# Performance work log

Measured on AMD Instinct MI355X. Metric: run time of the kernel, lower is better.

The kernel has to match this reference:

```python
import jax, jax.numpy as jnp
import numpy as np

B, S, HID = 2, 1024, 2048
N_HEADS, N_KV, HEAD_DIM = 32, 4, 128
BLOCK, MAX_BLOCKS = 32, 128
EPS = 1e-6
ROPE_THETA = 1e6


def _rmsnorm(x, w):
    # per-head RMSNorm over head_dim (Qwen3MoeRMSNorm)
    var = jnp.mean(x * x, axis=-1, keepdims=True)
    return x * jax.lax.rsqrt(var + EPS) * w


def _rotate_half(x):
    h = x.shape[-1] // 2
    return jnp.concatenate([-x[..., h:], x[..., :h]], axis=-1)


def setup_inputs() -> dict:
    key = jax.random.key(0)
    ks = jax.random.split(key, 8)
    hidden_states = jax.random.normal(ks[0], (B, S, HID), dtype=jnp.float32)
    wq = jax.random.normal(ks[1], (N_HEADS * HEAD_DIM, HID), dtype=jnp.float32) * 0.02
    wk = jax.random.normal(ks[2], (N_KV * HEAD_DIM, HID), dtype=jnp.float32) * 0.02
    wv = jax.random.normal(ks[3], (N_KV * HEAD_DIM, HID), dtype=jnp.float32) * 0.02
    wo = jax.random.normal(ks[4], (HID, N_HEADS * HEAD_DIM), dtype=jnp.float32) * 0.02
    q_norm_w = 1.0 + 0.01 * jax.random.normal(ks[5], (HEAD_DIM,), dtype=jnp.float32)
    k_norm_w = 1.0 + 0.01 * jax.random.normal(ks[6], (HEAD_DIM,), dtype=jnp.float32)
    # RoPE tables (rotate-half / llama convention)
    inv_freq = 1.0 / (ROPE_THETA ** (jnp.arange(0, HEAD_DIM, 2, dtype=jnp.float32) / HEAD_DIM))
    t = jnp.arange(S, dtype=jnp.float32)
    freqs = jnp.outer(t, inv_freq)  # [S, HEAD_DIM/2]
    emb = jnp.concatenate([freqs, freqs], axis=-1)  # [S, HEAD_DIM]
    cos, sin = jnp.cos(emb), jnp.sin(emb)
    # page table: B sequences x (S/BLOCK) blocks, distinct block ids
    page_table = jnp.arange(B * (S // BLOCK), dtype=jnp.int32).reshape(B, S // BLOCK)
    return {"hidden_states": hidden_states, "wq": wq, "wk": wk, "wv": wv, "wo": wo,
            "q_norm_w": q_norm_w, "k_norm_w": k_norm_w, "cos": cos, "sin": sin,
            "page_table": page_table}


def reference(hidden_states, wq, wk, wv, wo, q_norm_w, k_norm_w, cos, sin, page_table):
    b, s, _ = hidden_states.shape
    # fused QKV projection (math-equivalent to the concatenated qkv_proj_weight)
    q = (hidden_states @ wq.T).reshape(b, s, N_HEADS, HEAD_DIM)
    k = (hidden_states @ wk.T).reshape(b, s, N_KV, HEAD_DIM)
    v = (hidden_states @ wv.T).reshape(b, s, N_KV, HEAD_DIM)
    # per-head RMSNorm then RoPE
    q = _rmsnorm(q, q_norm_w)
    k = _rmsnorm(k, k_norm_w)
    c = cos[None, :, None, :]
    sn = sin[None, :, None, :]
    q = q * c + _rotate_half(q) * sn
    k = k * c + _rotate_half(k) * sn
    # paged KV-cache fill: [B, nblk, BLOCK, kvh, hd] -> cache[block_id, kvh, BLOCK, hd]
    nblk = s // BLOCK
    k_blk = k.reshape(b, nblk, BLOCK, N_KV, HEAD_DIM).transpose(0, 1, 3, 2, 4).reshape(-1, N_KV, BLOCK, HEAD_DIM)
    v_blk = v.reshape(b, nblk, BLOCK, N_KV, HEAD_DIM).transpose(0, 1, 3, 2, 4).reshape(-1, N_KV, BLOCK, HEAD_DIM)
    flat_pt = page_table.reshape(-1)
    cache_k = jnp.zeros((MAX_BLOCKS, N_KV, BLOCK, HEAD_DIM), dtype=k.dtype).at[flat_pt].set(k_blk)
    cache_v = jnp.zeros((MAX_BLOCKS, N_KV, BLOCK, HEAD_DIM), dtype=v.dtype).at[flat_pt].set(v_blk)
    # GQA: repeat kv heads (num_key_value_groups = 8)
    groups = N_HEADS // N_KV
    k_rep = jnp.repeat(k, groups, axis=2)  # [b, s, N_HEADS, hd]
    v_rep = jnp.repeat(v, groups, axis=2)
    # causal SDPA, scaling = head_dim ** -0.5
    scale = HEAD_DIM ** -0.5
    scores = jnp.einsum('bqhd,bkhd->bhqk', q, k_rep) * scale
    causal = jnp.tril(jnp.ones((s, s), dtype=bool))
    scores = jnp.where(causal[None, None], scores, jnp.finfo(scores.dtype).min)
    probs = jax.nn.softmax(scores, axis=-1)
    attn = jnp.einsum('bhqk,bkhd->bqhd', probs, v_rep).reshape(b, s, N_HEADS * HEAD_DIM)
    out = attn @ wo.T  # [b, s, HID]
    return out, cache_k, cache_v
```

## Files before the change

### kernel.cpp

```cpp
#include <hip/hip_runtime.h>
#include <hip/hip_bf16.h>


typedef __attribute__((ext_vector_type(8))) __bf16 bf16x8;
typedef __attribute__((ext_vector_type(4))) __bf16 bf16x4;
typedef __attribute__((ext_vector_type(4))) float f32x4;

__device__ __forceinline__ void gload16(const void* g, void* l) {
    __builtin_amdgcn_global_load_lds((const __attribute__((address_space(1))) void*)g,
                                     (__attribute__((address_space(3))) void*)l, 16, 0, 0);
}

__global__ __launch_bounds__(256) void cvt5(const float* __restrict__ s0, const float* __restrict__ s1,
                                            const float* __restrict__ s2, const float* __restrict__ s3,
                                            const float* __restrict__ s4,
                                            __bf16* __restrict__ d0, __bf16* __restrict__ d1,
                                            __bf16* __restrict__ d2, __bf16* __restrict__ d3,
                                            __bf16* __restrict__ d4) {
    const int b = blockIdx.x;
    const float* src; __bf16* dst; int off;
    if (b < 4096)       { src = s0; dst = d0; off = b; }
    else if (b < 12288) { src = s1; dst = d1; off = b - 4096; }
    else if (b < 13312) { src = s2; dst = d2; off = b - 12288; }
    else if (b < 14336) { src = s3; dst = d3; off = b - 13312; }
    else                { src = s4; dst = d4; off = b - 14336; }
    const int i = off * 256 + threadIdx.x;
    float4 v = reinterpret_cast<const float4*>(src)[i];
    bf16x4 o = {(__bf16)v.x, (__bf16)v.y, (__bf16)v.z, (__bf16)v.w};
    reinterpret_cast<bf16x4*>(dst)[i] = o;
}

__global__ __launch_bounds__(256) void reduce_add(float* __restrict__ o,
                                                  const float* __restrict__ p, int n4) {
    int i = blockIdx.x * 256 + threadIdx.x;
    int stride = gridDim.x * 256;
    for (; i < n4; i += stride) {
        float4 a = reinterpret_cast<float4*>(o)[i];
        float4 b = reinterpret_cast<const float4*>(p)[i];
        a.x += b.x; a.y += b.y; a.z += b.z; a.w += b.w;
        reinterpret_cast<float4*>(o)[i] = a;
    }
}

template <int NF, int OUT_BF16>
__global__ __launch_bounds__(512, 2) void gemm4p(const __bf16* __restrict__ A,
                                                 const __bf16* __restrict__ B,
                                                 void* __restrict__ C0,
                                                 void* __restrict__ C1,
                                                 const int M, const int N, const int K,
                                                 const int nTiles, const int nbn,
                                                 const int klen) {
    __shared__ __bf16 Asm[2 * 128 * 64];
    __shared__ __bf16 Bsm[2 * NF * 64 * 64];
    const int tid = threadIdx.x, lane = tid & 63, wave = tid >> 6;
    const int wm = wave >> 2, wn = wave & 3;
    const int lrow = lane & 15, lkg = lane >> 4;
    const int rsw = lrow & 7;
    const int bid = blockIdx.x;
    const int kz = bid / nTiles, tile = bid % nTiles;
    const int tswz = (tile & 7) * (nTiles >> 3) + (tile >> 3);
    const int bm = tswz / nbn, bn = tswz % nbn;
    const int brow = bm * 128, bcol = bn * (NF * 64);
    const int kbeg = kz * klen;
    const int row0 = tid >> 3;
    const int scol_sw = ((tid & 7) ^ (row0 & 7)) * 8;
    const __bf16* gA = A + (size_t)(brow + row0) * K + kbeg + scol_sw;
    const __bf16* gB = B + (size_t)(bcol + row0) * K + kbeg + scol_sw;
    const int slot0 = (lkg ^ rsw) * 8;
    const int slot1 = ((4 + lkg) ^ rsw) * 8;
    const int nt = klen / 64;
    constexpr int UPT = NF + 2;

    f32x4 acc[4][NF] = {};

    int su_t = 0, su_w = 0;
    auto stage1 = [&]() {
        if (su_t < nt) {
            const size_t ko = (size_t)su_t * 64;
            if (su_w < 2)
                gload16(gA + (size_t)(su_w * 64) * K + ko,
                        Asm + (su_t & 1) * 8192 + su_w * 4096 + tid * 8);
            else
                gload16(gB + (size_t)((su_w - 2) * 64) * K + ko,
                        Bsm + (su_t & 1) * (NF * 4096) + (su_w - 2) * 4096 + tid * 8);
        }
        if (++su_w == UPT) { su_w = 0; ++su_t; }
    };

    for (int u = 0; u < 2 * UPT; ++u) stage1();
    if constexpr (NF == 5) asm volatile("s_waitcnt vmcnt(7)" ::: "memory");
    else                   asm volatile("s_waitcnt vmcnt(6)" ::: "memory");
    __builtin_amdgcn_s_barrier();

    for (int t = 0; t < nt; ++t) {
        const __bf16* As = Asm + (t & 1) * 8192;
        const __bf16* Bs = Bsm + (t & 1) * (NF * 4096);
        bf16x8 ar[4], br[NF];
#pragma unroll
        for (int mi = 0; mi < 4; ++mi)
            ar[mi] = *reinterpret_cast<const bf16x8*>(&As[(wm * 64 + mi * 16 + lrow) * 64 + slot0]);
#pragma unroll
        for (int nf = 0; nf < NF; ++nf)
            br[nf] = *reinterpret_cast<const bf16x8*>(&Bs[(wn * (NF * 16) + nf * 16 + lrow) * 64 + slot0]);
        asm volatile("s_waitcnt lgkmcnt(0)" ::: "memory");
        __builtin_amdgcn_sched_barrier(0);
        __builtin_amdgcn_s_setprio(1);
#pragma unroll
        for (int mi = 0; mi < 4; ++mi)
#pragma unroll
            for (int nf = 0; nf < NF; ++nf)
                acc[mi][nf] = __builtin_amdgcn_mfma_f32_16x16x32_bf16(ar[mi], br[nf], acc[mi][nf], 0, 0, 0);
        __builtin_amdgcn_s_setprio(0);
        __builtin_amdgcn_s_barrier();
#pragma unroll
        for (int mi = 0; mi < 4; ++mi)
            ar[mi] = *reinterpret_cast<const bf16x8*>(&As[(wm * 64 + mi * 16 + lrow) * 64 + slot1]);
#pragma unroll
        for (int nf = 0; nf < NF; ++nf)
            br[nf] = *reinterpret_cast<const bf16x8*>(&Bs[(wn * (NF * 16) + nf * 16 + lrow) * 64 + slot1]);
        asm volatile("s_waitcnt lgkmcnt(0)" ::: "memory");
#pragma unroll
        for (int u = 0; u < UPT; ++u) stage1();
        __builtin_amdgcn_sched_barrier(0);
        __builtin_amdgcn_s_setprio(1);
#pragma unroll
        for (int mi = 0; mi < 4; ++mi)
#pragma unroll
            for (int nf = 0; nf < NF; ++nf)
                acc[mi][nf] = __builtin_amdgcn_mfma_f32_16x16x32_bf16(ar[mi], br[nf], acc[mi][nf], 0, 0, 0);
        __builtin_amdgcn_s_setprio(0);
        if (t + 2 < nt) {
            if constexpr (NF == 5) asm volatile("s_waitcnt vmcnt(7)" ::: "memory");
            else                   asm volatile("s_waitcnt vmcnt(6)" ::: "memory");
        } else {
            asm volatile("s_waitcnt vmcnt(0)" ::: "memory");
        }
        __builtin_amdgcn_s_barrier();
    }

    void* C = (kz == 0) ? C0 : C1;
#pragma unroll
    for (int mi = 0; mi < 4; ++mi)
#pragma unroll
        for (int nf = 0; nf < NF; ++nf)
#pragma unroll
            for (int j = 0; j < 4; ++j) {
                const size_t r = brow + wm * 64 + mi * 16 + lkg * 4 + j;
                const size_t c = bcol + wn * (NF * 16) + nf * 16 + lrow;
                if (OUT_BF16)
                    ((__bf16*)C)[r * N + c] = (__bf16)acc[mi][nf][j];
                else
                    ((float*)C)[r * N + c] = acc[mi][nf][j];
            }
}

__global__ __launch_bounds__(256) void norm_rope_cache(
    __bf16* __restrict__ qkv, const float* __restrict__ cosT, const float* __restrict__ sinT,
    const float* __restrict__ qw, const float* __restrict__ kw,
    const int* __restrict__ ptab, float* __restrict__ cacheK, float* __restrict__ cacheV) {
    const int t = blockIdx.x;
    const int b = t >> 10, s = t & 1023;
    const int wave = threadIdx.x >> 6, lane = threadIdx.x & 63;
    __bf16* row = qkv + (size_t)t * 5120;
    const float c = cosT[s * 128 + lane];
    const float sn = sinT[s * 128 + lane];
    const int page = ptab[b * 32 + (s >> 5)];
    const int so = s & 31;
    const float wq0 = qw[lane], wq1 = qw[lane + 64];
#pragma unroll
    for (int i = 0; i < 8; ++i) {
        const int h = wave * 8 + i;
        float x0 = (float)row[h * 128 + lane];
        float x1 = (float)row[h * 128 + 64 + lane];
        float ss = x0 * x0 + x1 * x1;
        for (int off = 32; off; off >>= 1) ss += __shfl_xor(ss, off);
        const float rs = rsqrtf(ss * (1.0f / 128.0f) + 1e-6f);
        const float y0 = x0 * rs * wq0, y1 = x1 * rs * wq1;
        row[h * 128 + lane]      = (__bf16)(y0 * c - y1 * sn);
        row[h * 128 + 64 + lane] = (__bf16)(y1 * c + y0 * sn);
    }
    {
        const int h = wave;
        float x0 = (float)row[4096 + h * 128 + lane];
        float x1 = (float)row[4096 + h * 128 + 64 + lane];
        float ss = x0 * x0 + x1 * x1;
        for (int off = 32; off; off >>= 1) ss += __shfl_xor(ss, off);
        const float rs = rsqrtf(ss * (1.0f / 128.0f) + 1e-6f);
        const float y0 = x0 * rs * kw[lane], y1 = x1 * rs * kw[lane + 64];
        const float o0 = y0 * c - y1 * sn, o1 = y1 * c + y0 * sn;
        row[4096 + h * 128 + lane]      = (__bf16)o0;
        row[4096 + h * 128 + 64 + lane] = (__bf16)o1;
        float* ck = cacheK + (((size_t)page * 4 + h) * 32 + so) * 128;
        ck[lane] = o0; ck[lane + 64] = o1;
        const float v0 = (float)row[4608 + h * 128 + lane];
        const float v1 = (float)row[4608 + h * 128 + 64 + lane];
        float* cv = cacheV + (((size_t)page * 4 + h) * 32 + so) * 128;
        cv[lane] = v0; cv[lane + 64] = v1;
    }
}

__global__ __launch_bounds__(512, 2) void attn_fwd(const __bf16* __restrict__ qkv,
                                                   __bf16* __restrict__ out) {
    __shared__ __bf16 Ks[2][128 * 128];
    __shared__ __bf16 Vs[128 * 128];
    __shared__ __bf16 Ps[8][2][16 * 64];
    const int bid = blockIdx.x;
    const int qa = bid >> 3;
    const int g = bid & 7;
    const int kvg = g & 3, b = g >> 2;
    const int qbig = 63 - qa;
    const int tid = threadIdx.x, wave = tid >> 6, lane = tid & 63;
    const int lrow = lane & 15, lkg = lane >> 4;
    const int h = kvg * 8 + wave;
    const size_t base = (size_t)b * 1024 * 5120;
    const int kofs = 4096 + kvg * 128, vofs = 4608 + kvg * 128;
    const int ntA = qa / 8 + 1, nt = qbig / 8 + 1;
    const int lastA = qa >> 2, lastB = qbig >> 2;
    const int qposA = qa * 16 + lrow, qposB = qbig * 16 + lrow;
    const int rsw = lrow & 7;
    constexpr float QS = 0.08838834764831845f * 1.4426950408889634f;
    constexpr float SUB = 20.0f;

    bf16x8 aqA[4], aqB[4];
#pragma unroll
    for (int kc = 0; kc < 4; ++kc) {
        bf16x8 ta = *reinterpret_cast<const bf16x8*>(
            &qkv[base + (size_t)(qa * 16 + lrow) * 5120 + h * 128 + kc * 32 + lkg * 8]);
        bf16x8 tb = *reinterpret_cast<const bf16x8*>(
            &qkv[base + (size_t)(qbig * 16 + lrow) * 5120 + h * 128 + kc * 32 + lkg * 8]);
#pragma unroll
        for (int i = 0; i < 8; ++i) {
            ta[i] = (__bf16)((float)ta[i] * QS);
            tb[i] = (__bf16)((float)tb[i] * QS);
        }
        aqA[kc] = ta; aqB[kc] = tb;
    }

    f32x4 accA[8] = {}, accB[8] = {};
    float lA = 0.f, lB = 0.f;
    __bf16* PwA = &Ps[wave][0][0];
    __bf16* PwB = &Ps[wave][1][0];

    auto stageK = [&](int t, int buf) {
        const int kv0 = (t < nt) ? t * 128 : 0;
#pragma unroll
        for (int c = 0; c < 4; ++c) {
            const int chunk = c * 8 + wave;
            const int row = chunk * 4 + (lane >> 4);
            const int gslot = (lane & 15) ^ (row & 7);
            gload16(&qkv[base + (size_t)(kv0 + row) * 5120 + kofs + gslot * 8],
                    &Ks[buf][chunk * 512]);
        }
    };
    auto loadV = [&](int t, uint4 (&vr)[4]) {
        const int kv0 = (t < nt) ? t * 128 : 0;
#pragma unroll
        for (int r = 0; r < 4; ++r) {
            const int kv = (r & 1) * 64 + lane;
            const int d0 = wave * 16 + (r >> 1) * 8;
            vr[r] = *reinterpret_cast<const uint4*>(
                &qkv[base + (size_t)(kv0 + kv) * 5120 + vofs + d0]);
        }
    };
    auto writeV = [&](uint4 (&vr)[4]) {
#pragma unroll
        for (int r = 0; r < 4; ++r) {
            const __bf16* pv = reinterpret_cast<const __bf16*>(&vr[r]);
            const int kv = (r & 1) * 64 + lane;
            const int slot = kv >> 3, klo = kv & 7;
#pragma unroll
            for (int j = 0; j < 8; ++j) {
                const int d = wave * 16 + (r >> 1) * 8 + j;
                Vs[d * 128 + ((slot ^ (d & 7)) << 3) + klo] = pv[j];
            }
        }
    };

    auto smax = [&](f32x4 (&st)[4], float& l_lane, int qpos, int kv0, bool maskit, __bf16* Pw) {
#pragma unroll
        for (int f = 0; f < 4; ++f) {
            bf16x4 pb;
#pragma unroll
            for (int j = 0; j < 4; ++j) {
                float x = st[f][j];
                if (maskit) {
                    const int kvpos = kv0 + f * 16 + lkg * 4 + j;
                    if (kvpos > qpos) x = -1e30f;
                }
                const float p = exp2f(x - SUB);
                l_lane += p;
                pb[j] = (__bf16)p;
            }
            const int slot = (f * 2 + (lkg >> 1)) ^ rsw;
            *reinterpret_cast<bf16x4*>(&Pw[lrow * 64 + slot * 8 + (lkg & 1) * 4]) = pb;
        }
    };

    auto pvH = [&](f32x4 (&acc)[8], int hf, __bf16* Pw) {
#pragma unroll
        for (int kk = 0; kk < 2; ++kk) {
            const int pslot = ((kk * 4 + lkg) ^ rsw) << 3;
            bf16x8 ap = *reinterpret_cast<const bf16x8*>(&Pw[lrow * 64 + pslot]);
#pragma unroll
            for (int f = 0; f < 8; ++f) {
                bf16x8 bv = *reinterpret_cast<const bf16x8*>(
                    &Vs[(f * 16 + lrow) * 128 + hf * 64 + pslot]);
                acc[f] = __builtin_amdgcn_mfma_f32_16x16x32_bf16(ap, bv, acc[f], 0, 0, 0);
            }
        }
    };

    auto body = [&](int t, uint4 (&vcur)[4], uint4 (&vnext)[4]) {
        const int kbuf = t & 1;
        __builtin_amdgcn_s_barrier();
        asm volatile("" ::: "memory");
        loadV(t + 1, vnext);
        stageK(t + 1, kbuf ^ 1);
        asm volatile("s_waitcnt vmcnt(8)" ::: "memory");
        writeV(vcur);
        asm volatile("s_waitcnt lgkmcnt(0)" ::: "memory");
        __builtin_amdgcn_s_barrier();
        asm volatile("" ::: "memory");

        const bool doA = t < ntA;
#pragma unroll
        for (int hf = 0; hf < 2; ++hf) {
            const int kh = 2 * t + hf;
            const bool actA = doA && (kh <= lastA);
            const bool actB = kh <= lastB;
            if (!actB && !actA) continue;
            f32x4 stA[4] = {}, stB[4] = {};
#pragma unroll
            for (int kc = 0; kc < 4; ++kc)
#pragma unroll
                for (int f = 0; f < 4; ++f) {
                    bf16x8 ak = *reinterpret_cast<const bf16x8*>(
                        &Ks[kbuf][(hf * 64 + f * 16 + lrow) * 128 + (((kc * 4 + lkg) ^ rsw) << 3)]);
                    if (actB)
                        stB[f] = __builtin_amdgcn_mfma_f32_16x16x32_bf16(ak, aqB[kc], stB[f], 0, 0, 0);
                    if (actA)
                        stA[f] = __builtin_amdgcn_mfma_f32_16x16x32_bf16(ak, aqA[kc], stA[f], 0, 0, 0);
                }
            const int kv0 = t * 128 + hf * 64;
            if (actA) {
                smax(stA, lA, qposA, kv0, kh == lastA, PwA);
                pvH(accA, hf, PwA);
            }
            if (actB) {
                smax(stB, lB, qposB, kv0, kh == lastB, PwB);
                pvH(accB, hf, PwB);
            }
        }
    };

    uint4 vrA[4], vrB[4];
    loadV(0, vrA);
    stageK(0, 0);
    for (int t = 0; t < nt; t += 2) {
        body(t, vrA, vrB);
        if (t + 1 < nt) body(t + 1, vrB, vrA);
    }
    asm volatile("s_waitcnt vmcnt(0)" ::: "memory");

    lA += __shfl_xor(lA, 16); lA += __shfl_xor(lA, 32);
    lB += __shfl_xor(lB, 16); lB += __shfl_xor(lB, 32);
    float linvA[4], linvB[4];
#pragma unroll
    for (int j = 0; j < 4; ++j) {
        linvA[j] = 1.0f / __shfl(lA, lkg * 4 + j);
        linvB[j] = 1.0f / __shfl(lB, lkg * 4 + j);
    }
#pragma unroll
    for (int f = 0; f < 8; ++f)
#pragma unroll
        for (int j = 0; j < 4; ++j) {
            out[((size_t)b * 1024 + qa * 16 + lkg * 4 + j) * 4096 + h * 128 + f * 16 + lrow] =
                (__bf16)(accA[f][j] * linvA[j]);
            out[((size_t)b * 1024 + qbig * 16 + lkg * 4 + j) * 4096 + h * 128 + f * 16 + lrow] =
                (__bf16)(accB[f][j] * linvB[j]);
        }
}

extern "C" void kernel_launch(void* const* d_in, const int* in_sizes, int n_in,
                              void* d_out, int out_size, void* d_ws, size_t ws_size,
                              hipStream_t stream) {
    const float* hidden = (const float*)d_in[0];
    const float* wq = (const float*)d_in[1];
    const float* wk = (const float*)d_in[2];
    const float* wv = (const float*)d_in[3];
    const float* wo = (const float*)d_in[4];
    const float* qnw = (const float*)d_in[5];
    const float* knw = (const float*)d_in[6];
    const float* cosT = (const float*)d_in[7];
    const float* sinT = (const float*)d_in[8];
    const int* ptab = (const int*)d_in[9];

    float* outp = (float*)d_out;
    float* cacheK = outp + 4194304;
    float* cacheV = cacheK + 2097152;

    char* ws = (char*)d_ws;
    __bf16* hbf    = (__bf16*)ws;
    __bf16* w1bf   = (__bf16*)(ws + 8388608);
    __bf16* wobf   = (__bf16*)(ws + 29360128);
    __bf16* qkvbf  = (__bf16*)(ws + 46137344);
    __bf16* attnbf = (__bf16*)ws;
    float*  opart  = (float*)(ws + 46137344);

    cvt5<<<22528, 256, 0, stream>>>(hidden, wq, wk, wv, wo,
                                    hbf, w1bf, w1bf + (size_t)4096 * 2048,
                                    w1bf + (size_t)4608 * 2048, wobf);

    gemm4p<5, 1><<<256, 512, 0, stream>>>(hbf, w1bf, qkvbf, nullptr,
                                          2048, 5120, 2048, 256, 16, 2048);

    hipMemsetAsync(cacheK, 0, (size_t)4194304 * 4, stream);
    norm_rope_cache<<<2048, 256, 0, stream>>>(qkvbf, cosT, sinT, qnw, knw, ptab, cacheK, cacheV);

    attn_fwd<<<256, 512, 0, stream>>>(qkvbf, attnbf);

    gemm4p<4, 0><<<256, 512, 0, stream>>>(attnbf, wobf, outp, opart,
                                          2048, 2048, 4096, 128, 8, 2048);
    reduce_add<<<2048, 256, 0, stream>>>(outp, opart, 4194304 / 4);
}
```

Baseline: 191.3 us.

## Share V fragment loads across both query tiles and pack V LDS writes

The attention kernel now runs the PV MFMAs for both query tiles (A and B) in one loop, so each V fragment read from LDS is reused by two accumulators instead of being loaded twice. V rows are read as adjacent kv pairs so two bf16 values can be written to LDS as one 32-bit store, halving LDS write instructions. The launch bound drops to one block per SIMD group, giving the compiler more registers at the cost of occupancy. The convert kernel also handles two float4 per thread with half the grid, cutting block launch overhead.

```diff
diff --git a/kernel.cpp b/kernel.cpp
--- a/kernel.cpp
+++ b/kernel.cpp
@@ -19,15 +19,18 @@
                                             __bf16* __restrict__ d4) {
     const int b = blockIdx.x;
     const float* src; __bf16* dst; int off;
-    if (b < 4096)       { src = s0; dst = d0; off = b; }
-    else if (b < 12288) { src = s1; dst = d1; off = b - 4096; }
-    else if (b < 13312) { src = s2; dst = d2; off = b - 12288; }
-    else if (b < 14336) { src = s3; dst = d3; off = b - 13312; }
-    else                { src = s4; dst = d4; off = b - 14336; }
-    const int i = off * 256 + threadIdx.x;
-    float4 v = reinterpret_cast<const float4*>(src)[i];
-    bf16x4 o = {(__bf16)v.x, (__bf16)v.y, (__bf16)v.z, (__bf16)v.w};
-    reinterpret_cast<bf16x4*>(dst)[i] = o;
+    if (b < 2048)      { src = s0; dst = d0; off = b; }
+    else if (b < 6144) { src = s1; dst = d1; off = b - 2048; }
+    else if (b < 6656) { src = s2; dst = d2; off = b - 6144; }
+    else if (b < 7168) { src = s3; dst = d3; off = b - 6656; }
+    else               { src = s4; dst = d4; off = b - 7168; }
+#pragma unroll
+    for (int u = 0; u < 2; ++u) {
+        const int i = off * 512 + u * 256 + threadIdx.x;
+        float4 v = reinterpret_cast<const float4*>(src)[i];
+        bf16x4 o = {(__bf16)v.x, (__bf16)v.y, (__bf16)v.z, (__bf16)v.w};
+        reinterpret_cast<bf16x4*>(dst)[i] = o;
+    }
 }
 
 __global__ __launch_bounds__(256) void reduce_add(float* __restrict__ o,
@@ -199,7 +202,7 @@
     }
 }
 
-__global__ __launch_bounds__(512, 2) void attn_fwd(const __bf16* __restrict__ qkv,
+__global__ __launch_bounds__(512, 1) void attn_fwd(const __bf16* __restrict__ qkv,
                                                    __bf16* __restrict__ out) {
     __shared__ __bf16 Ks[2][128 * 128];
     __shared__ __bf16 Vs[128 * 128];
@@ -256,22 +259,25 @@
         const int kv0 = (t < nt) ? t * 128 : 0;
 #pragma unroll
         for (int r = 0; r < 4; ++r) {
-            const int kv = (r & 1) * 64 + lane;
+            const int kv = 2 * lane + (r & 1);
             const int d0 = wave * 16 + (r >> 1) * 8;
             vr[r] = *reinterpret_cast<const uint4*>(
                 &qkv[base + (size_t)(kv0 + kv) * 5120 + vofs + d0]);
         }
     };
     auto writeV = [&](uint4 (&vr)[4]) {
-#pragma unroll
-        for (int r = 0; r < 4; ++r) {
-            const __bf16* pv = reinterpret_cast<const __bf16*>(&vr[r]);
-            const int kv = (r & 1) * 64 + lane;
-            const int slot = kv >> 3, klo = kv & 7;
+        const int slot = lane >> 2;
+        const int klo = (2 * lane) & 7;
+#pragma unroll
+        for (int hh = 0; hh < 2; ++hh) {
+            const unsigned short* e0 = reinterpret_cast<const unsigned short*>(&vr[2 * hh]);
+            const unsigned short* e1 = reinterpret_cast<const unsigned short*>(&vr[2 * hh + 1]);
 #pragma unroll
             for (int j = 0; j < 8; ++j) {
-                const int d = wave * 16 + (r >> 1) * 8 + j;
-                Vs[d * 128 + ((slot ^ (d & 7)) << 3) + klo] = pv[j];
+                const int d = wave * 16 + hh * 8 + j;
+                const unsigned val = (unsigned)e0[j] | ((unsigned)e1[j] << 16);
+                *reinterpret_cast<unsigned*>(
+                    &Vs[d * 128 + ((slot ^ (d & 7)) << 3) + klo]) = val;
             }
         }
     };
@@ -296,16 +302,21 @@
         }
     };
 
-    auto pvH = [&](f32x4 (&acc)[8], int hf, __bf16* Pw) {
+    auto pvBoth = [&](int hf, bool actA, bool actB) {
 #pragma unroll
         for (int kk = 0; kk < 2; ++kk) {
             const int pslot = ((kk * 4 + lkg) ^ rsw) << 3;
-            bf16x8 ap = *reinterpret_cast<const bf16x8*>(&Pw[lrow * 64 + pslot]);
+            bf16x8 apA = {}, apB = {};
+            if (actA) apA = *reinterpret_cast<const bf16x8*>(&PwA[lrow * 64 + pslot]);
+            if (actB) apB = *reinterpret_cast<const bf16x8*>(&PwB[lrow * 64 + pslot]);
 #pragma unroll
             for (int f = 0; f < 8; ++f) {
                 bf16x8 bv = *reinterpret_cast<const bf16x8*>(
                     &Vs[(f * 16 + lrow) * 128 + hf * 64 + pslot]);
-                acc[f] = __builtin_amdgcn_mfma_f32_16x16x32_bf16(ap, bv, acc[f], 0, 0, 0);
+                if (actA)
+                    accA[f] = __builtin_amdgcn_mfma_f32_16x16x32_bf16(apA, bv, accA[f], 0, 0, 0);
+                if (actB)
+                    accB[f] = __builtin_amdgcn_mfma_f32_16x16x32_bf16(apB, bv, accB[f], 0, 0, 0);
             }
         }
     };
@@ -342,14 +353,9 @@
                         stA[f] = __builtin_amdgcn_mfma_f32_16x16x32_bf16(ak, aqA[kc], stA[f], 0, 0, 0);
                 }
             const int kv0 = t * 128 + hf * 64;
-            if (actA) {
-                smax(stA, lA, qposA, kv0, kh == lastA, PwA);
-                pvH(accA, hf, PwA);
-            }
-            if (actB) {
-                smax(stB, lB, qposB, kv0, kh == lastB, PwB);
-                pvH(accB, hf, PwB);
-            }
+            if (actA) smax(stA, lA, qposA, kv0, kh == lastA, PwA);
+            if (actB) smax(stB, lB, qposB, kv0, kh == lastB, PwB);
+            pvBoth(hf, actA, actB);
         }
     };
 
@@ -407,7 +413,7 @@
     __bf16* attnbf = (__bf16*)ws;
     float*  opart  = (float*)(ws + 46137344);
 
-    cvt5<<<22528, 256, 0, stream>>>(hidden, wq, wk, wv, wo,
+    cvt5<<<11264, 256, 0, stream>>>(hidden, wq, wk, wv, wo,
                                     hbf, w1bf, w1bf + (size_t)4096 * 2048,
                                     w1bf + (size_t)4608 * 2048, wobf);
 
```

After: 193.2 us. No clear change (+1.0%).
